# Kernel tuning notes

Measured on AMD Instinct MI355X. Metric: run time of the kernel, lower is better.

Reference implementation:

```python
import jax, jax.numpy as jnp
import numpy as np
from jax import lax

NH = 8  # heads


def _ln(x, g, b):
    m = x.mean(-1, keepdims=True)
    v = ((x - m) ** 2).mean(-1, keepdims=True)
    return (x - m) * lax.rsqrt(v + 1e-5) * g + b


def _pos_idx(n):
    # torch: linspace(n-1,0,n)[:,None] + linspace(0,n-1,n)[None,:], flattened long
    r = np.linspace(n - 1, 0, n).reshape(n, 1)
    c = np.linspace(0, n - 1, n).reshape(1, n)
    return jnp.asarray((r + c).reshape(-1).astype(np.int32))


def _mha(q_in, k_in, v_in, in_w, in_b, out_w, out_b, pos_enc=None, pos_idx=None, attn_mask=None):
    # MultiheadAttentionRelative: q/k/v proj + relative pos-encoding gather terms
    w, bsz, e = q_in.shape
    hd = e // NH
    scale = hd ** -0.5
    q = (q_in @ in_w[:e].T + in_b[:e]) * scale
    k = k_in @ in_w[e:2 * e].T + in_b[e:2 * e]
    v = v_in @ in_w[2 * e:].T + in_b[2 * e:]
    q = q.reshape(w, bsz, NH, hd)
    k = k.reshape(w, bsz, NH, hd)
    v = v.reshape(w, bsz, NH, hd)
    attn = jnp.einsum('wnec,vnec->newv', q, k)  # [N,E,W,W']
    if pos_enc is not None:
        pe = pos_enc[pos_idx].reshape(w, w, e)  # [2W-1,C] -> [W,W',C] gather
        q_r = ((pe @ in_w[:e].T + in_b[:e]) * scale).reshape(w, w, NH, hd)
        k_r = (pe @ in_w[e:2 * e].T + in_b[e:2 * e]).reshape(w, w, NH, hd)
        attn = attn + jnp.einsum('wnec,wvec->newv', q, k_r) + jnp.einsum('vnec,wvec->newv', k, q_r)
    if attn_mask is not None:
        attn = attn + attn_mask[None, None]
    raw = attn
    p = jax.nn.softmax(attn, axis=-1)
    v_o = jnp.einsum('newv,vnec->wnec', p, v).reshape(w, bsz, e)
    return v_o @ out_w.T + out_b, raw.sum(axis=1)


def _interp_lin(x, out_size):
    # torch F.interpolate(mode='linear', align_corners=False) along last axis
    L_in = x.shape[-1]
    if L_in == out_size:
        return x
    coords = jnp.clip((jnp.arange(out_size, dtype=jnp.float32) + 0.5) * (L_in / out_size) - 0.5, 0.0, L_in - 1.0)
    lo = jnp.floor(coords).astype(jnp.int32)
    hi = jnp.minimum(lo + 1, L_in - 1)
    frac = coords - lo.astype(jnp.float32)
    return x[..., lo] * (1.0 - frac) + x[..., hi] * frac


def _conv(x, w, b, pad):
    y = lax.conv_general_dilated(x, w, (1, 1), pad, dimension_numbers=('NCHW', 'OIHW', 'NCHW'))
    return y + b[None, :, None, None]


def _self_layer(feat, feat1, pos, pidx, pos1, pidx1, posy, pidxy, posy1, pidxy1, p):
    iw, ib, ow, ob, n1g, n1b, n2g, n2b = p
    f2 = _ln(feat, n1g, n1b)
    f4 = _ln(feat1, n2g, n2b)
    w_, h2, c = f2.shape
    w1_, h4, c1 = f4.shape
    # row<->col switch: [W,2HN,C] -> [HN,2W,C]
    f2y = jnp.transpose(f2.reshape(w_, 2, h2 // 2, c), (2, 1, 0, 3)).reshape(h2 // 2, 2 * w_, c)
    f4y = jnp.transpose(f4.reshape(w1_, 2, h4 // 2, c1), (2, 1, 0, 3)).reshape(h4 // 2, 2 * w1_, c1)
    f2y, _ = _mha(f2y, f2y, f2y, iw[1], ib[1], ow[1], ob[1], posy, pidxy)
    f2 = jnp.transpose(f2y.reshape(h2 // 2, 2, w_, c), (2, 1, 0, 3)).reshape(w_, h2, c)
    f4y, _ = _mha(f4y, f4y, f4y, iw[3], ib[3], ow[3], ob[3], posy1, pidxy1)
    f4 = jnp.transpose(f4y.reshape(h4 // 2, 2, w1_, c1), (2, 1, 0, 3)).reshape(w1_, h4, c1)
    f2, _ = _mha(f2, f2, f2, iw[0], ib[0], ow[0], ob[0], pos, pidx)
    f4, _ = _mha(f4, f4, f4, iw[2], ib[2], ow[2], ob[2], pos1, pidx1)
    return feat + f2, feat1 + f4


def _cross_layer(fl, fr, fl1, fr1, pos, pidx, pos1, pidx1, p, last):
    iw, ib, ow, ob, n1g, n1b, n2g, n2b, mw1, mb1, mw2, mb2 = p
    fl2 = _ln(fl, n1g, n1b)
    fr2 = _ln(fr, n1g, n1b)
    fl4 = _ln(fl1, n2g, n2b)
    fr4 = _ln(fr1, n2g, n2b)
    up_r, _ = _mha(fr2, fl2, fl2, iw[0], ib[0], ow[0], ob[0], jnp.flip(pos, 0), pidx)
    up_r1, _ = _mha(fr4, fl4, fl4, iw[1], ib[1], ow[1], ob[1], jnp.flip(pos1, 0), pidx1)
    fr = fr + up_r
    fr1n = fr1 + up_r1
    if last:
        w = fl2.shape[0]
        w1 = fl4.shape[0]
        m = jnp.where(jnp.triu(jnp.ones((w, w), jnp.float32), 1) == 1.0, -jnp.inf, 0.0)
        m1 = jnp.where(jnp.triu(jnp.ones((w1, w1), jnp.float32), 1) == 1.0, -jnp.inf, 0.0)
    else:
        m = None
        m1 = None
    fr2n = _ln(fr, n1g, n1b)
    up_l, raw = _mha(fl2, fr2n, fr2n, iw[0], ib[0], ow[0], ob[0], pos, pidx, m)
    fr4n = _ln(fr1n, n2g, n2b)
    up_l1, _ = _mha(fl4, fr4n, fr4n, iw[1], ib[1], ow[1], ob[1], pos1, pidx1, m1)
    fl = fl + up_l
    fl1n = fl1 + up_l1
    feat = jnp.concatenate([fl, fr], 1)        # [W,2HN,C]
    feat_n = jnp.concatenate([fl1n, fr1n], 1)  # [W1,2HN,C]
    x = jnp.transpose(feat_n, (2, 1, 0))       # [C,2HN,W1]
    x = _interp_lin(x, feat.shape[0])          # [C,2HN,W]
    feat_n = jnp.transpose(x, (2, 1, 0))
    feat_n = jnp.concatenate([feat_n, feat], 2)  # [W,2HN,2C]
    x = jnp.transpose(feat_n, (2, 1, 0))[None]   # [1,2C,2HN,W]
    x = _conv(x, mw1, mb1, 'VALID')
    x = _conv(x, mw2, mb2, ((1, 1), (1, 1)))
    out = jnp.transpose(x[0], (2, 1, 0))         # [W,2HN,C]
    return out, raw


def reference(feat_left, feat_right, feat_left1, feat_right1, pos_enc, pos_enc1, pos_enc_y, pos_enc_y1,
              sa_in_w, sa_in_b, sa_out_w, sa_out_b, sa_n1_g, sa_n1_b, sa_n2_g, sa_n2_b,
              ca_in_w, ca_in_b, ca_out_w, ca_out_b, ca_n1_g, ca_n1_b, ca_n2_g, ca_n2_b,
              merge_w1, merge_b1, merge_w2, merge_b2):
    bs, c, h, w = feat_left.shape
    w1 = feat_left1.shape[3]
    hn = h * bs

    def flat(x):
        return jnp.transpose(x, (3, 2, 0, 1)).reshape(x.shape[3], -1, c)  # [W,HN,C]

    fl, fr = flat(feat_left), flat(feat_right)
    fl1, fr1 = flat(feat_left1), flat(feat_right1)
    pidx = _pos_idx(w)
    pidx1 = _pos_idx(w1)
    pidxy = _pos_idx(hn)
    pidxy1 = _pos_idx(hn)
    feat = jnp.concatenate([fl, fr], 1)    # [W,2HN,C]
    feat1 = jnp.concatenate([fl1, fr1], 1)  # [W1,2HN,C]
    L = sa_in_w.shape[0]
    raw = None
    for i in range(L):
        sp = (sa_in_w[i], sa_in_b[i], sa_out_w[i], sa_out_b[i], sa_n1_g[i], sa_n1_b[i], sa_n2_g[i], sa_n2_b[i])
        feat, feat1 = _self_layer(feat, feat1, pos_enc, pidx, pos_enc1, pidx1, pos_enc_y, pidxy, pos_enc_y1, pidxy1, sp)
        cp = (ca_in_w[i], ca_in_b[i], ca_out_w[i], ca_out_b[i], ca_n1_g[i], ca_n1_b[i], ca_n2_g[i], ca_n2_b[i],
              merge_w1[i], merge_b1[i], merge_w2[i], merge_b2[i])
        feat, raw = _cross_layer(feat[:, :hn], feat[:, hn:], feat1[:, :hn], feat1[:, hn:],
                                 pos_enc, pidx, pos_enc1, pidx1, cp, i == L - 1)
    attn_weight = jnp.transpose(raw.reshape(h, bs, w, w), (1, 0, 2, 3))  # [N,H,W,W]
    return attn_weight


def setup_inputs() -> dict:
    key = jax.random.key(0)
    ks = iter(jax.random.split(key, 40))
    N, C, H, W, W1, Lyr = 1, 128, 64, 128, 64, 6
    s = 0.05
    d = {}
    d['feat_left'] = jax.random.normal(next(ks), (N, C, H, W), jnp.float32)
    d['feat_right'] = jax.random.normal(next(ks), (N, C, H, W), jnp.float32)
    d['feat_left1'] = jax.random.normal(next(ks), (N, C, H, W1), jnp.float32)
    d['feat_right1'] = jax.random.normal(next(ks), (N, C, H, W1), jnp.float32)
    d['pos_enc'] = jax.random.normal(next(ks), (2 * W - 1, C), jnp.float32) * 0.1
    d['pos_enc1'] = jax.random.normal(next(ks), (2 * W1 - 1, C), jnp.float32) * 0.1
    d['pos_enc_y'] = jax.random.normal(next(ks), (2 * H - 1, C), jnp.float32) * 0.1
    d['pos_enc_y1'] = jax.random.normal(next(ks), (2 * H - 1, C), jnp.float32) * 0.1
    d['sa_in_w'] = jax.random.normal(next(ks), (Lyr, 4, 3 * C, C), jnp.float32) * s
    d['sa_in_b'] = jnp.zeros((Lyr, 4, 3 * C), jnp.float32)
    d['sa_out_w'] = jax.random.normal(next(ks), (Lyr, 4, C, C), jnp.float32) * s
    d['sa_out_b'] = jnp.zeros((Lyr, 4, C), jnp.float32)
    d['sa_n1_g'] = jnp.ones((Lyr, C), jnp.float32)
    d['sa_n1_b'] = jnp.zeros((Lyr, C), jnp.float32)
    d['sa_n2_g'] = jnp.ones((Lyr, C), jnp.float32)
    d['sa_n2_b'] = jnp.zeros((Lyr, C), jnp.float32)
    d['ca_in_w'] = jax.random.normal(next(ks), (Lyr, 2, 3 * C, C), jnp.float32) * s
    d['ca_in_b'] = jnp.zeros((Lyr, 2, 3 * C), jnp.float32)
    d['ca_out_w'] = jax.random.normal(next(ks), (Lyr, 2, C, C), jnp.float32) * s
    d['ca_out_b'] = jnp.zeros((Lyr, 2, C), jnp.float32)
    d['ca_n1_g'] = jnp.ones((Lyr, C), jnp.float32)
    d['ca_n1_b'] = jnp.zeros((Lyr, C), jnp.float32)
    d['ca_n2_g'] = jnp.ones((Lyr, C), jnp.float32)
    d['ca_n2_b'] = jnp.zeros((Lyr, C), jnp.float32)
    d['merge_w1'] = jax.random.normal(next(ks), (Lyr, 128, 256, 1, 1), jnp.float32) * s
    d['merge_b1'] = jnp.zeros((Lyr, 128), jnp.float32)
    d['merge_w2'] = jax.random.normal(next(ks), (Lyr, 128, 128, 3, 3), jnp.float32) * s
    d['merge_b2'] = jnp.zeros((Lyr, 128), jnp.float32)
    return d
```

## Files before the change

### kernel.cpp

```cpp
#include <hip/hip_runtime.h>
#include <hip/hip_bf16.h>
#include <math.h>


typedef __attribute__((ext_vector_type(8))) short bf16x8;
typedef __attribute__((ext_vector_type(4))) float f32x4;
typedef __hip_bfloat16 bf16;

__device__ __forceinline__ float b2f(unsigned short u) {
  return __uint_as_float((unsigned)u << 16);
}
__device__ __forceinline__ short f2bs(float x) {
  bf16 h = __float2bfloat16(x);
  short s;
  __builtin_memcpy(&s, &h, 2);
  return s;
}
__device__ __forceinline__ int ymap(int t, int D0, int D1) {
  return (t % D0) * (2 * D1) + ((t / D0) & 1) * D1 + t / (2 * D0);
}


__global__ void k_build_feat(const float* __restrict__ L, const float* __restrict__ R,
                             float* __restrict__ feat, int W) {
  int t = blockIdx.x;
  int c = threadIdx.x;
  int b = t & 127;
  int w = t >> 7;
  const float* src = (b < 64) ? L : R;
  int h = b & 63;
  feat[(size_t)t * 128 + c] = src[((size_t)c * 64 + h) * W + w];
}

struct FDesc { const float* s; bf16* d; int n; };
struct FArgs { FDesc d[9]; int cum[10]; int nprob; };
__global__ void k_f2b_multi(FArgs fa) {
  int bid = blockIdx.x;
  int p = 0;
  while (p + 1 < fa.nprob && bid >= fa.cum[p + 1]) ++p;
  const FDesc d = fa.d[p];
  int i = (bid - fa.cum[p]) * 1024 + threadIdx.x * 4;
  if (i + 3 < d.n) {
    float4 x = *(const float4*)(d.s + i);
    d.d[i + 0] = __float2bfloat16(x.x);
    d.d[i + 1] = __float2bfloat16(x.y);
    d.d[i + 2] = __float2bfloat16(x.z);
    d.d[i + 3] = __float2bfloat16(x.w);
  } else {
    for (int z = 0; z < 4 && i + z < d.n; ++z) d.d[i + z] = __float2bfloat16(d.s[i + z]);
  }
}

__global__ void k_wfullb(const float* __restrict__ w2, bf16* __restrict__ wf) {
  int bid = blockIdx.x;
  int l = bid >> 7, co = bid & 127;
  int ci = threadIdx.x;
  const float* src = w2 + (size_t)l * 128 * 128 * 9;
  bf16* dst = wf + (size_t)l * 128 * 1152;
#pragma unroll
  for (int ky = 0; ky < 3; ky++)
#pragma unroll
    for (int kx = 0; kx < 3; kx++)
      dst[(size_t)co * 1152 + (kx * 3 + ky) * 128 + ci] =
          __float2bfloat16(src[((size_t)(co * 128 + ci) * 3 + ky) * 3 + kx]);
}

__global__ void k_zero_guard(bf16* p0, bf16* p1) {
  int t = threadIdx.x;
  p0[255 * 256 + t] = __float2bfloat16(0.0f);
  p1[127 * 256 + t] = __float2bfloat16(0.0f);
}

__global__ void k_rawcomb4(const float* __restrict__ A, const float* __restrict__ B2,
                           const float* __restrict__ C3, const float* __restrict__ D4,
                           bf16* __restrict__ out) {
  int i = blockIdx.x * 256 + threadIdx.x;
  int v = i & 127, w = (i >> 7) & 127;
  float rv = (v > w) ? 0.0f : (A[i] + B2[i] + C3[i] + D4[i]);
  out[i] = __float2bfloat16(rv);
}


struct LDesc { const float* src; bf16* dst; const float* g; const float* be;
               int ntok, Bout, PBin, offIn; };
struct LArgs { LDesc d[4]; int cum[5]; int nprob; };

__global__ __launch_bounds__(256) void k_ln_multi(LArgs la) {
  int bid = blockIdx.x;
  int p = 0;
  while (p + 1 < la.nprob && bid >= la.cum[p + 1]) ++p;
  const LDesc d = la.d[p];
  int t = (bid - la.cum[p]) * 4 + (threadIdx.x >> 6);
  int lane = threadIdx.x & 63;
  if (t >= d.ntok) return;
  int w = t / d.Bout, b = t - w * d.Bout;
  const float* row = d.src + (size_t)(w * d.PBin + d.offIn + b) * 128;
  float x0 = row[lane], x1 = row[lane + 64];
  float s = x0 + x1;
#pragma unroll
  for (int o = 32; o; o >>= 1) s += __shfl_xor(s, o, 64);
  float m = s * (1.0f / 128.0f);
  float d0 = x0 - m, d1 = x1 - m;
  float v = d0 * d0 + d1 * d1;
#pragma unroll
  for (int o = 32; o; o >>= 1) v += __shfl_xor(v, o, 64);
  float r = 1.0f / sqrtf(v * (1.0f / 128.0f) + 1e-5f);
  bf16* orow = d.dst + (size_t)t * 128;
  orow[lane]      = __float2bfloat16(d0 * r * d.g[lane]      + d.be[lane]);
  orow[lane + 64] = __float2bfloat16(d1 * r * d.g[lane + 64] + d.be[lane + 64]);
}


struct GDesc {
  const bf16* A; const float* Af0; const float* Af1;
  const bf16* W; const float* bias;
  bf16* Cb; float* Cf; const float* resid;
  int M, N, K, lda, scaleN;
  int imode, iD0, iD1;
  int omode, oD0, oD1, ooff;
};
struct GArgs { GDesc d[6]; int cum[7]; int nprob; };

__global__ __launch_bounds__(256) void k_gemm_multi(GArgs ga) {
  __shared__ bf16x8 sA[64 * 4];
  __shared__ bf16x8 sB[64 * 4];
  int bid = blockIdx.x;
  int p = 0;
  while (p + 1 < ga.nprob && bid >= ga.cum[p + 1]) ++p;
  const GDesc d = ga.d[p];
  int local = bid - ga.cum[p];
  int tilesx = d.N >> 6;
  int ty = local / tilesx, tx = local - ty * tilesx;
  const int m0 = ty << 6, n0 = tx << 6;
  const int tid = threadIdx.x;
  const int lane = tid & 63;
  const int wave = tid >> 6;
  const int wm = wave >> 1, wn = wave & 1;
  const int fr = lane & 15;
  const int kc = lane >> 4;
  f32x4 acc[2][2];
#pragma unroll
  for (int f = 0; f < 2; f++)
#pragma unroll
    for (int g = 0; g < 2; g++) acc[f][g] = (f32x4){0.f, 0.f, 0.f, 0.f};

  for (int k0 = 0; k0 < d.K; k0 += 32) {
    {
      int row = tid >> 2, ch = tid & 3;
      int m = m0 + row;
      bf16x8 val = (bf16x8){0, 0, 0, 0, 0, 0, 0, 0};
      if (d.imode == 0) {
        if (m < d.M) val = *(const bf16x8*)(d.A + (size_t)m * d.lda + k0 + ch * 8);
      } else if (d.imode == 1) {
        if (m < d.M) {
          int ar = ymap(m, d.iD0, d.iD1);
          val = *(const bf16x8*)(d.A + (size_t)ar * d.lda + k0 + ch * 8);
        }
      } else if (d.imode == 2) {
        int kblk = k0 >> 7;
        int kx = kblk / 3, ky = kblk - kx * 3;
        int arow = m + (kx - 1) * 128;
        int y = (m & 127) + (ky - 1);
        if (arow >= 0 && arow < d.M && y >= 0 && y < 128)
          val = *(const bf16x8*)(d.A + (size_t)arow * d.lda + (k0 & 127) + ch * 8);
      } else {
        int kk = k0 + ch * 8;
        int w = m >> 7, y = m & 127;
        if (kk < 128) {
          float xo = fminf(fmaxf(w * 0.5f - 0.25f, 0.0f), 63.0f);
          int lo = (int)xo;
          int hi = (lo + 1 < 63) ? lo + 1 : 63;
          float f = xo - (float)lo;
          const float* a0 = d.Af0 + ((size_t)lo * 128 + y) * 128 + kk;
          const float* a1 = d.Af0 + ((size_t)hi * 128 + y) * 128 + kk;
#pragma unroll
          for (int z = 0; z < 8; ++z) val[z] = f2bs(a0[z] * (1.0f - f) + a1[z] * f);
        } else {
          const float* a0 = d.Af1 + (size_t)m * 128 + (kk - 128);
#pragma unroll
          for (int z = 0; z < 8; ++z) val[z] = f2bs(a0[z]);
        }
      }
      sA[row * 4 + (ch ^ ((row >> 2) & 3))] = val;
      bf16x8 bval = *(const bf16x8*)(d.W + (size_t)(n0 + row) * d.K + k0 + ch * 8);
      sB[row * 4 + (ch ^ ((row >> 2) & 3))] = bval;
    }
    __syncthreads();
    bf16x8 af[2], bg[2];
#pragma unroll
    for (int f = 0; f < 2; ++f) {
      int row = wm * 32 + f * 16 + fr;
      af[f] = sA[row * 4 + (kc ^ ((row >> 2) & 3))];
    }
#pragma unroll
    for (int g = 0; g < 2; ++g) {
      int row = wn * 32 + g * 16 + fr;
      bg[g] = sB[row * 4 + (kc ^ ((row >> 2) & 3))];
    }
#pragma unroll
    for (int f = 0; f < 2; ++f)
#pragma unroll
      for (int g = 0; g < 2; ++g)
        acc[f][g] = __builtin_amdgcn_mfma_f32_16x16x32_bf16(af[f], bg[g], acc[f][g], 0, 0, 0);
    __syncthreads();
  }
  const int r4 = (lane >> 4) << 2;
  const int ocol = lane & 15;
#pragma unroll
  for (int f = 0; f < 2; ++f) {
#pragma unroll
    for (int g = 0; g < 2; ++g) {
      int n = n0 + wn * 32 + g * 16 + ocol;
      float bv = d.bias ? d.bias[n] : 0.0f;
      bool sc = (n < d.scaleN);
#pragma unroll
      for (int i = 0; i < 4; ++i) {
        int m = m0 + wm * 32 + f * 16 + r4 + i;
        if (m < d.M) {
          int row;
          if (d.omode == 0) row = (m / d.oD0) * d.oD1 + d.ooff + (m % d.oD0);
          else row = ymap(m, d.oD0, d.oD1);
          size_t idx = (size_t)row * d.N + n;
          float val = acc[f][g][i] + bv;
          if (sc) val *= 0.25f;
          if (d.resid) val += d.resid[idx];
          if (d.Cb) d.Cb[idx] = __float2bfloat16(val);
          else d.Cf[idx] = val;
        }
      }
    }
  }
}


struct ADesc {
  const bf16* Q; const bf16* K; const bf16* V;
  const bf16* PPb; bf16* O;
  float* raw0; float* raw1; float* raw2; float* raw3;
  int ldQ, ldK, ldV, Wlen, B, sflip, useMask;
};
struct AArgs { ADesc d[2]; int cum[3]; int nprob; };

template<int WLEN, int SGN>
__device__ __forceinline__ void attn_core(const ADesc& d, int b, int st, int h,
                                          int tid, bf16* Vt, bf16* Pl, bf16* T2l,
                                          bf16* Ost) {
  constexpr int NT = WLEN / 16;
  constexpr int R = WLEN - 1;
  const f32x4 z4 = (f32x4){0.f, 0.f, 0.f, 0.f};
  const bf16x8 zb = (bf16x8){0, 0, 0, 0, 0, 0, 0, 0};

  {
    int q = tid & (WLEN / 2 - 1);
    int cc = tid >> ((WLEN == 128) ? 6 : 5);
    constexpr int CH = (WLEN == 128) ? 16 : 8;
    int cb = cc * CH;
    const bf16* v0p = d.V + ((size_t)(2 * q) * d.B + b) * d.ldV + h * 64 + cb;
    const bf16* v1p = d.V + ((size_t)(2 * q + 1) * d.B + b) * d.ldV + h * 64 + cb;
#pragma unroll
    for (int j = 0; j < CH; j += 8) {
      bf16x8 a = *(const bf16x8*)(v0p + j);
      bf16x8 bb = *(const bf16x8*)(v1p + j);
#pragma unroll
      for (int z = 0; z < 8; ++z) {
        unsigned pk = (unsigned)(unsigned short)a[z] |
                      ((unsigned)(unsigned short)bb[z] << 16);
        *(unsigned*)(Vt + (size_t)(cb + j + z) * 136 + 2 * q) = pk;
      }
    }
  }
  __syncthreads();

  const int wave = tid >> 6, l = tid & 63;
  const int lm = l & 15, lg = l >> 4;
  const bool zlane = (lg >= 2);
  bf16* Pw  = Pl + wave * (16 * 136);
  bf16* T2w = T2l + wave * (16 * 20);
  int p0[4], src[4], hi[4], tsel[4];
  bool csel[4];
#pragma unroll
  for (int i = 0; i < 4; ++i) {
    p0[i] = SGN * (lm - 4 * lg - i) + 15;
    src[i] = (l & 48) | (p0[i] & 15);
    hi[i] = p0[i] & 16;
    if (SGN == 1) {
      int t0 = lm + 15 - 4 * lg - i;
      csel[i] = (t0 < 16);
      tsel[i] = csel[i] ? t0 : t0 - 16;
    } else {
      int t0 = lm - 15 + 4 * lg + i;
      csel[i] = (t0 >= 0);
      tsel[i] = csel[i] ? t0 : t0 + 16;
    }
  }

  const int w0 = st * 16;
  const int chb = h * 64 + wave * 16 + lg * 8;

  bf16x8 qf = zb;
  if (!zlane) qf = *(const bf16x8*)(d.Q + ((size_t)(w0 + lm) * d.B + b) * d.ldQ + chb);

  const int U0 = (SGN == 1) ? (R - w0 - 15) : (R + w0 - WLEN + 1);
  const int Ub0 = (SGN == 1) ? (R - w0 - 15) : (R - (WLEN - 16) + w0 - 15);
  const bf16* t1p = d.PPb + (size_t)(U0 + lm) * 256 + 128 + chb;
  const bf16* t2p = d.PPb + (size_t)(Ub0 + lm) * 256 + chb;
  const int v0i = ((SGN == 1) ? 0 : (WLEN - 16)) + lm;
  const bf16* kp = d.K + ((size_t)v0i * d.B + b) * d.ldK + chb;
  const ptrdiff_t kstep = (ptrdiff_t)SGN * 16 * d.B * d.ldK;

  f32x4 t1a;
  {
    bf16x8 z = zb;
    if (!zlane) z = *(const bf16x8*)t1p;
    t1p += 16 * 256;
    t1a = __builtin_amdgcn_mfma_f32_16x16x32_bf16(qf, z, z4, 0, 0, 0);
  }
  int v = v0i;
#pragma unroll
  for (int j = 0; j < NT; ++j) {
    f32x4 t1b;
    {
      bf16x8 z = zb;
      if (!zlane) z = *(const bf16x8*)t1p;
      t1p += 16 * 256;
      t1b = __builtin_amdgcn_mfma_f32_16x16x32_bf16(qf, z, z4, 0, 0, 0);
    }
    bf16x8 kf = zb;
    if (!zlane) kf = *(const bf16x8*)kp;
    kp += kstep;
    f32x4 s4 = __builtin_amdgcn_mfma_f32_16x16x32_bf16(qf, kf, z4, 0, 0, 0);
    bf16x8 zA = zb, zB = zb;
    if (!zlane) {
      zA = *(const bf16x8*)t2p;
      zB = *(const bf16x8*)(t2p + 16 * 256);
    }
    t2p += 16 * 256;
    f32x4 t2A = __builtin_amdgcn_mfma_f32_16x16x32_bf16(zA, kf, z4, 0, 0, 0);
    f32x4 t2B = __builtin_amdgcn_mfma_f32_16x16x32_bf16(zB, kf, z4, 0, 0, 0);
#pragma unroll
    for (int i = 0; i < 4; ++i)
      T2w[lm * 20 + tsel[i]] = f2bs(csel[i] ? t2A[i] : t2B[i]);
    ushort4 t2u = *(const ushort4*)(T2w + lm * 20 + 4 * lg);
    unsigned short t2a[4] = {t2u.x, t2u.y, t2u.z, t2u.w};
#pragma unroll
    for (int i = 0; i < 4; ++i) {
      float va = __shfl(t1a[i], src[i], 64);
      float vb = __shfl(t1b[i], src[i], 64);
      float s = s4[i] + (hi[i] ? vb : va) + b2f(t2a[i]);
      Pw[(4 * lg + i) * 136 + v] = f2bs(__expf(s));
    }
    t1a = t1b;
    v += SGN * 16;
  }
  const bf16x8 ones = (bf16x8){0x3F80, 0x3F80, 0x3F80, 0x3F80,
                               0x3F80, 0x3F80, 0x3F80, 0x3F80};
  f32x4 oa = z4, rsm = z4;
#pragma unroll
  for (int vc = 0; vc < NT / 2; ++vc) {
    bf16x8 pf = *(const bf16x8*)(Pw + lm * 136 + vc * 32 + lg * 8);
    bf16x8 vf = *(const bf16x8*)(Vt + (size_t)(wave * 16 + lm) * 136 + vc * 32 + lg * 8);
    oa = __builtin_amdgcn_mfma_f32_16x16x32_bf16(pf, vf, oa, 0, 0, 0);
    rsm = __builtin_amdgcn_mfma_f32_16x16x32_bf16(pf, ones, rsm, 0, 0, 0);
  }
#pragma unroll
  for (int i = 0; i < 4; ++i)
    Ost[(4 * lg + i) * 80 + wave * 16 + lm] = f2bs(oa[i] / rsm[i]);
  __syncthreads();
  if (tid < 128) {
    int row = tid >> 3, ch8 = (tid & 7) * 8;
    bf16x8 vv = *(const bf16x8*)(Ost + row * 80 + ch8);
    *(bf16x8*)(d.O + ((size_t)(w0 + row) * d.B + b) * 128 + h * 64 + ch8) = vv;
  }
}

__global__ __launch_bounds__(256, 4) void k_attn_mfma(AArgs aa) {
  __shared__ bf16 Vt[64 * 136];
  __shared__ bf16 Pl[4 * 16 * 136];
  __shared__ bf16 T2l[4 * 16 * 20];
  __shared__ bf16 Ost[16 * 80];
  int bid = blockIdx.x;
  int p = 0;
  while (p + 1 < aa.nprob && bid >= aa.cum[p + 1]) ++p;
  const ADesc d = aa.d[p];
  int local = bid - aa.cum[p];
  int b = local % d.B;
  int rest = local / d.B;
  int ns = d.Wlen >> 4;
  int st = rest % ns, h = rest / ns;
  int tid = threadIdx.x;
  if (d.Wlen == 128) {
    if (d.sflip == 1) attn_core<128, 1>(d, b, st, h, tid, Vt, Pl, T2l, Ost);
    else attn_core<128, -1>(d, b, st, h, tid, Vt, Pl, T2l, Ost);
  } else {
    if (d.sflip == 1) attn_core<64, 1>(d, b, st, h, tid, Vt, Pl, T2l, Ost);
    else attn_core<64, -1>(d, b, st, h, tid, Vt, Pl, T2l, Ost);
  }
}

__global__ __launch_bounds__(256, 2) void k_attn_raw(ADesc d) {
  __shared__ bf16 T2l[4 * 16 * 20];
  constexpr int NT = 8;
  constexpr int R = 127;
  const f32x4 z4 = (f32x4){0.f, 0.f, 0.f, 0.f};
  const bf16x8 zb = (bf16x8){0, 0, 0, 0, 0, 0, 0, 0};
  int bid = blockIdx.x;
  int b = bid % d.B, st = bid / d.B;
  int tid = threadIdx.x;
  const int wave = tid >> 6, l = tid & 63;
  const int lm = l & 15, lg = l >> 4;
  const bool zlane = (lg >= 2);
  bf16* T2w = T2l + wave * (16 * 20);
  int p0[4];
#pragma unroll
  for (int i = 0; i < 4; ++i) p0[i] = (lm - 4 * lg - i) + 15;
  const int w0 = st * 16;
  f32x4 raw[NT];
#pragma unroll
  for (int vt = 0; vt < NT; ++vt) raw[vt] = z4;

  for (int hh = 0; hh < 2; ++hh) {
    const int e = wave * 2 + hh;
    const int chb = e * 16 + lg * 8;
    bf16x8 qf = zb;
    if (!zlane) qf = *(const bf16x8*)(d.Q + ((size_t)(w0 + lm) * d.B + b) * d.ldQ + chb);
    const int U0 = R - w0 - 15;
    f32x4 t1a;
    {
      int u = min(max(U0 + lm, 0), 2 * R);
      bf16x8 z = zb;
      if (!zlane) z = *(const bf16x8*)(d.PPb + (size_t)u * 256 + 128 + chb);
      t1a = __builtin_amdgcn_mfma_f32_16x16x32_bf16(qf, z, z4, 0, 0, 0);
    }
#pragma unroll
    for (int j = 0; j < NT; ++j) {
      const int vt = j;
      const int v = vt * 16 + lm;
      f32x4 t1b;
      {
        int u = min(max(U0 + (j + 1) * 16 + lm, 0), 2 * R);
        bf16x8 z = zb;
        if (!zlane) z = *(const bf16x8*)(d.PPb + (size_t)u * 256 + 128 + chb);
        t1b = __builtin_amdgcn_mfma_f32_16x16x32_bf16(qf, z, z4, 0, 0, 0);
      }
      bf16x8 kf = zb;
      if (!zlane) kf = *(const bf16x8*)(d.K + ((size_t)v * d.B + b) * d.ldK + chb);
      f32x4 s4 = __builtin_amdgcn_mfma_f32_16x16x32_bf16(qf, kf, z4, 0, 0, 0);
      const int Ub = R + vt * 16 - w0 - 15;
#pragma unroll
      for (int u2 = 0; u2 < 2; ++u2) {
        int ua = min(max(Ub + u2 * 16 + lm, 0), 2 * R);
        bf16x8 z = zb;
        if (!zlane) z = *(const bf16x8*)(d.PPb + (size_t)ua * 256 + chb);
        f32x4 t2 = __builtin_amdgcn_mfma_f32_16x16x32_bf16(z, kf, z4, 0, 0, 0);
#pragma unroll
        for (int i = 0; i < 4; ++i) {
          int u = Ub + u2 * 16 + 4 * lg + i;
          int t = R + v - u - w0;
          if (t >= 0 && t < 16) T2w[lm * 20 + t] = f2bs(t2[i]);
        }
      }
      ushort4 t2u = *(const ushort4*)(T2w + lm * 20 + 4 * lg);
      unsigned short t2a[4] = {t2u.x, t2u.y, t2u.z, t2u.w};
#pragma unroll
      for (int i = 0; i < 4; ++i) {
        int src = (l & 48) | (p0[i] & 15);
        float va = __shfl(t1a[i], src, 64);
        float vb = __shfl(t1b[i], src, 64);
        float s = s4[i] + ((p0[i] & 16) ? vb : va) + b2f(t2a[i]);
        if (v > (w0 + 4 * lg + i)) s = -INFINITY;
        raw[vt][i] += s;
      }
      t1a = t1b;
    }
  }
  float* rp = (wave == 0) ? d.raw0 : (wave == 1) ? d.raw1 : (wave == 2) ? d.raw2 : d.raw3;
#pragma unroll
  for (int vt = 0; vt < NT; ++vt)
#pragma unroll
    for (int i = 0; i < 4; ++i)
      rp[((size_t)b * 128 + (w0 + 4 * lg + i)) * 128 + vt * 16 + lm] = raw[vt][i];
}


extern "C" void kernel_launch(void* const* d_in, const int* in_sizes, int n_in,
                              void* d_out, int out_size, void* d_ws, size_t ws_size,
                              hipStream_t stream) {
  (void)in_sizes; (void)n_in; (void)out_size; (void)ws_size;
  const float* FLt  = (const float*)d_in[0];
  const float* FRt  = (const float*)d_in[1];
  const float* FL1t = (const float*)d_in[2];
  const float* FR1t = (const float*)d_in[3];
  const float* PE   = (const float*)d_in[4];
  const float* PE1  = (const float*)d_in[5];
  const float* PEY  = (const float*)d_in[6];
  const float* PEY1 = (const float*)d_in[7];
  const float* SA_IW = (const float*)d_in[8];
  const float* SA_IB = (const float*)d_in[9];
  const float* SA_OW = (const float*)d_in[10];
  const float* SA_OB = (const float*)d_in[11];
  const float* SA_N1G = (const float*)d_in[12];
  const float* SA_N1B = (const float*)d_in[13];
  const float* SA_N2G = (const float*)d_in[14];
  const float* SA_N2B = (const float*)d_in[15];
  const float* CA_IW = (const float*)d_in[16];
  const float* CA_IB = (const float*)d_in[17];
  const float* CA_OW = (const float*)d_in[18];
  const float* CA_OB = (const float*)d_in[19];
  const float* CA_N1G = (const float*)d_in[20];
  const float* CA_N1B = (const float*)d_in[21];
  const float* CA_N2G = (const float*)d_in[22];
  const float* CA_N2B = (const float*)d_in[23];
  const float* MW1 = (const float*)d_in[24];
  const float* MB1 = (const float*)d_in[25];
  const float* MW2 = (const float*)d_in[26];
  const float* MB2 = (const float*)d_in[27];

  float* ws = (float*)d_ws;
  float* FEAT  = ws;
  float* FEAT1 = ws + 2097152;
  float* FN2   = ws + 3145728;
  bf16* PP0b   = (bf16*)(ws + 4194304);
  bf16* PP1b   = (bf16*)(ws + 4259840);
  bf16* hb = (bf16*)(ws + 4292608);
  bf16* QKV   = hb;
  bf16* QKV1  = hb + 6291456;
  bf16* Xb    = hb + 9437184;
  bf16* XBb   = hb + 11534336;
  bf16* Ob    = hb + 12582912;
  bf16* Ob1   = hb + 14680064;
  bf16* PEb   = hb + 15728640;
  bf16* PE1b  = hb + 15761408;
  bf16* PEYb  = hb + 15777792;
  bf16* PEY1b = hb + 15794176;
  bf16* SAIWb = hb + 15810560;
  bf16* SAOWb = hb + 18169856;
  bf16* CAIWb = hb + 18563072;
  bf16* CAOWb = hb + 19742720;
  bf16* MW1b  = hb + 19939328;
  bf16* WFb   = hb + 20135936;

  bf16* QR   = QKV + 3145728;
  bf16* FL4F = QKV + 4194304;
  bf16* QR1  = QKV + 5767168;
  bf16* KVq  = QKV1;
  bf16* KVq1 = QKV1 + 2097152;
  bf16* XR2  = Xb;
  bf16* XR21 = Xb + 1048576;

  GArgs ga; int ng = 0; int gb = 0;
  auto gadd = [&](GDesc gd) { ga.cum[ng] = gb; ga.d[ng] = gd;
                              gb += ((gd.M + 63) >> 6) * (gd.N >> 6); ++ng; };
  auto gflush = [&]() { ga.nprob = ng;
                        k_gemm_multi<<<gb, 256, 0, stream>>>(ga); ng = 0; gb = 0; };
  LArgs la; int nl = 0; int lb = 0;
  auto lnadd = [&](LDesc ld) { la.cum[nl] = lb; la.d[nl] = ld;
                               lb += (ld.ntok + 3) / 4; ++nl; };
  auto lnflush = [&]() { la.nprob = nl;
                         k_ln_multi<<<lb, 256, 0, stream>>>(la); nl = 0; lb = 0; };
  AArgs aa; int na = 0; int ab = 0;
  auto aadd = [&](ADesc ad) { aa.cum[na] = ab; aa.d[na] = ad;
                              ab += ad.B * (ad.Wlen >> 4) * 2; ++na; };
  auto aflush = [&]() { aa.nprob = na;
                        k_attn_mfma<<<ab, 256, 0, stream>>>(aa); na = 0; ab = 0; };

  auto G = [&](const bf16* A, const bf16* W, const float* bias,
               bf16* Cb, float* Cf, const float* resid,
               int M, int N, int K, int lda, int scaleN,
               int imode, int iD0, int iD1,
               int omode, int oD0, int oD1, int ooff,
               const float* Af0 = nullptr, const float* Af1 = nullptr) {
    GDesc gd; gd.A = A; gd.Af0 = Af0; gd.Af1 = Af1; gd.W = W; gd.bias = bias;
    gd.Cb = Cb; gd.Cf = Cf; gd.resid = resid;
    gd.M = M; gd.N = N; gd.K = K; gd.lda = lda; gd.scaleN = scaleN;
    gd.imode = imode; gd.iD0 = iD0; gd.iD1 = iD1;
    gd.omode = omode; gd.oD0 = oD0; gd.oD1 = oD1; gd.ooff = ooff;
    gadd(gd);
  };
  auto AT = [&](const bf16* Q, int ldQ, const bf16* K, int ldK, const bf16* V, int ldV,
                const bf16* PPb, int Wlen, int B, int sflip, bf16* O) {
    ADesc ad; ad.Q = Q; ad.K = K; ad.V = V; ad.PPb = PPb; ad.O = O;
    ad.raw0 = nullptr; ad.raw1 = nullptr; ad.raw2 = nullptr; ad.raw3 = nullptr;
    ad.ldQ = ldQ; ad.ldK = ldK; ad.ldV = ldV; ad.Wlen = Wlen; ad.B = B;
    ad.sflip = sflip; ad.useMask = 0;
    aadd(ad);
  };

  {
    FArgs fa; int nf = 0; int fb = 0;
    auto fadd = [&](const float* s, bf16* dd, int n) {
      fa.cum[nf] = fb; fa.d[nf] = FDesc{s, dd, n}; fb += (n + 1023) / 1024; ++nf; };
    fadd(SA_IW, SAIWb, 6 * 4 * 384 * 128);
    fadd(SA_OW, SAOWb, 6 * 4 * 128 * 128);
    fadd(CA_IW, CAIWb, 6 * 2 * 384 * 128);
    fadd(CA_OW, CAOWb, 6 * 2 * 128 * 128);
    fadd(MW1,   MW1b,  6 * 128 * 256);
    fadd(PE,    PEb,   255 * 128);
    fadd(PE1,   PE1b,  127 * 128);
    fadd(PEY,   PEYb,  127 * 128);
    fadd(PEY1,  PEY1b, 127 * 128);
    fa.nprob = nf;
    k_f2b_multi<<<fb, 256, 0, stream>>>(fa);
  }
  k_wfullb<<<768, 128, 0, stream>>>(MW2, WFb);
  k_zero_guard<<<1, 256, 0, stream>>>(PP0b, PP1b);
  k_build_feat<<<16384, 128, 0, stream>>>(FLt, FRt, FEAT, 128);
  k_build_feat<<<8192, 128, 0, stream>>>(FL1t, FR1t, FEAT1, 64);

  for (int l = 0; l < 6; ++l) {
    bool last = (l == 5);
    const bf16* iw  = SAIWb + (size_t)l * 4 * 384 * 128;
    const float* ib = SA_IB + (size_t)l * 4 * 384;
    const bf16* ow  = SAOWb + (size_t)l * 4 * 128 * 128;
    const float* ob = SA_OB + (size_t)l * 4 * 128;
    const bf16* ciw  = CAIWb + (size_t)l * 2 * 384 * 128;
    const float* cib = CA_IB + (size_t)l * 2 * 384;
    const bf16* cow  = CAOWb + (size_t)l * 2 * 128 * 128;
    const float* cob = CA_OB + (size_t)l * 2 * 128;
    const bf16* ciw1 = ciw + 384 * 128;
    const float* cib1 = cib + 384;
    const bf16* cow1 = cow + 128 * 128;
    const float* cob1 = cob + 128;
    const int IW = 384 * 128, OW = 128 * 128;

    lnadd(LDesc{FEAT, Xb, SA_N1G + l * 128, SA_N1B + l * 128, 16384, 128, 128, 0});
    if (!last) lnadd(LDesc{FEAT1, XBb, SA_N2G + l * 128, SA_N2B + l * 128, 8192, 128, 128, 0});
    lnflush();
    G(Xb, iw + IW, ib + 384, QKV, nullptr, nullptr, 16384, 384, 128, 128, 128, 1, 128, 64, 0, 1, 1, 0);
    if (!last) G(XBb, iw + 3 * IW, ib + 3 * 384, QKV1, nullptr, nullptr, 8192, 384, 128, 128, 128, 1, 64, 64, 0, 1, 1, 0);
    G(PEYb, iw + IW, ib + 384, PP0b, nullptr, nullptr, 127, 256, 128, 128, 128, 0, 0, 0, 0, 1, 1, 0);
    if (!last) G(PEY1b, iw + 3 * IW, ib + 3 * 384, PP1b, nullptr, nullptr, 127, 256, 128, 128, 128, 0, 0, 0, 0, 1, 1, 0);
    gflush();
    AT(QKV, 384, QKV + 128, 384, QKV + 256, 384, PP0b, 64, 256, 1, Ob);
    if (!last) AT(QKV1, 384, QKV1 + 128, 384, QKV1 + 256, 384, PP1b, 64, 128, 1, Ob1);
    aflush();
    G(Ob, ow + OW, ob + 128, Xb, nullptr, nullptr, 16384, 128, 128, 128, 0, 0, 0, 0, 1, 128, 64, 0);
    if (!last) G(Ob1, ow + 3 * OW, ob + 3 * 128, XBb, nullptr, nullptr, 8192, 128, 128, 128, 0, 0, 0, 0, 1, 64, 64, 0);
    gflush();
    G(Xb, iw, ib, QKV, nullptr, nullptr, 16384, 384, 128, 128, 128, 0, 0, 0, 0, 1, 1, 0);
    if (!last) G(XBb, iw + 2 * IW, ib + 2 * 384, QKV1, nullptr, nullptr, 8192, 384, 128, 128, 128, 0, 0, 0, 0, 1, 1, 0);
    G(PEb, iw, ib, PP0b, nullptr, nullptr, 255, 256, 128, 128, 128, 0, 0, 0, 0, 1, 1, 0);
    if (!last) G(PE1b, iw + 2 * IW, ib + 2 * 384, PP1b, nullptr, nullptr, 127, 256, 128, 128, 128, 0, 0, 0, 0, 1, 1, 0);
    gflush();
    AT(QKV, 384, QKV + 128, 384, QKV + 256, 384, PP0b, 128, 128, 1, Ob);
    if (!last) AT(QKV1, 384, QKV1 + 128, 384, QKV1 + 256, 384, PP1b, 64, 128, 1, Ob1);
    aflush();
    G(Ob, ow, ob, nullptr, FEAT, FEAT, 16384, 128, 128, 128, 0, 0, 0, 0, 0, 1, 1, 0);
    if (!last) G(Ob1, ow + 2 * OW, ob + 2 * 128, nullptr, FEAT1, FEAT1, 8192, 128, 128, 128, 0, 0, 0, 0, 0, 1, 1, 0);
    gflush();

    lnadd(LDesc{FEAT, Xb, CA_N1G + l * 128, CA_N1B + l * 128, 8192, 64, 128, 0});
    lnadd(LDesc{FEAT, Xb + 1048576, CA_N1G + l * 128, CA_N1B + l * 128, 8192, 64, 128, 64});
    if (!last) {
      lnadd(LDesc{FEAT1, XBb, CA_N2G + l * 128, CA_N2B + l * 128, 4096, 64, 128, 0});
      lnadd(LDesc{FEAT1, XBb + 524288, CA_N2G + l * 128, CA_N2B + l * 128, 4096, 64, 128, 64});
    }
    lnflush();
    G(Xb, ciw, cib, QKV, nullptr, nullptr, 8192, 384, 128, 128, 128, 0, 0, 0, 0, 1, 1, 0);
    G(Xb + 1048576, ciw, cib, QR, nullptr, nullptr, 8192, 128, 128, 128, 128, 0, 0, 0, 0, 1, 1, 0);
    if (!last) {
      G(XBb, ciw1, cib1, FL4F, nullptr, nullptr, 4096, 384, 128, 128, 128, 0, 0, 0, 0, 1, 1, 0);
      G(XBb + 524288, ciw1, cib1, QR1, nullptr, nullptr, 4096, 128, 128, 128, 128, 0, 0, 0, 0, 1, 1, 0);
    }
    G(PEb, ciw, cib, PP0b, nullptr, nullptr, 255, 256, 128, 128, 128, 0, 0, 0, 0, 1, 1, 0);
    if (!last) G(PE1b, ciw1, cib1, PP1b, nullptr, nullptr, 127, 256, 128, 128, 128, 0, 0, 0, 0, 1, 1, 0);
    gflush();
    AT(QR, 128, QKV + 128, 384, QKV + 256, 384, PP0b, 128, 64, -1, Ob);
    if (!last) AT(QR1, 128, FL4F + 128, 384, FL4F + 256, 384, PP1b, 64, 64, -1, Ob1);
    aflush();
    G(Ob, cow, cob, nullptr, FEAT, FEAT, 8192, 128, 128, 128, 0, 0, 0, 0, 0, 64, 128, 64);
    if (!last) G(Ob1, cow1, cob1, nullptr, FN2, FEAT1, 4096, 128, 128, 128, 0, 0, 0, 0, 0, 64, 128, 64);
    gflush();
    lnadd(LDesc{FEAT, XR2, CA_N1G + l * 128, CA_N1B + l * 128, 8192, 64, 128, 64});
    if (!last) lnadd(LDesc{FN2, XR21, CA_N2G + l * 128, CA_N2B + l * 128, 4096, 64, 128, 64});
    lnflush();
    G(XR2, ciw + 128 * 128, cib + 128, KVq, nullptr, nullptr, 8192, 256, 128, 128, 0, 0, 0, 0, 0, 1, 1, 0);
    if (!last) G(XR21, ciw1 + 128 * 128, cib1 + 128, KVq1, nullptr, nullptr, 4096, 256, 128, 128, 0, 0, 0, 0, 0, 1, 1, 0);
    gflush();
    if (last) {
      ADesc ad; ad.Q = QKV; ad.K = KVq; ad.V = KVq + 128; ad.PPb = PP0b;
      ad.O = nullptr;
      ad.raw0 = FEAT1; ad.raw1 = FN2; ad.raw2 = (float*)Ob; ad.raw3 = (float*)FL4F;
      ad.ldQ = 384; ad.ldK = 256; ad.ldV = 256;
      ad.Wlen = 128; ad.B = 64; ad.sflip = 1; ad.useMask = 1;
      k_attn_raw<<<64 * 8, 256, 0, stream>>>(ad);
      k_rawcomb4<<<4096, 256, 0, stream>>>(FEAT1, FN2, (float*)Ob, (float*)FL4F,
                                           (bf16*)d_out);
      break;
    }
    AT(QKV, 384, KVq, 256, KVq + 128, 256, PP0b, 128, 64, 1, Ob);
    AT(FL4F, 384, KVq1, 256, KVq1 + 128, 256, PP1b, 64, 64, 1, Ob1);
    aflush();
    G(Ob, cow, cob, nullptr, FEAT, FEAT, 8192, 128, 128, 128, 0, 0, 0, 0, 0, 64, 128, 0);
    G(Ob1, cow1, cob1, nullptr, FN2, FEAT1, 4096, 128, 128, 128, 0, 0, 0, 0, 0, 64, 128, 0);
    gflush();
    G(nullptr, MW1b + (size_t)l * 128 * 256, MB1 + l * 128, Ob, nullptr, nullptr,
      16384, 128, 256, 256, 0, 3, 0, 0, 0, 1, 1, 0, FN2, FEAT);
    gflush();
    G(Ob, WFb + (size_t)l * 128 * 1152, MB2 + l * 128, nullptr, FEAT, nullptr,
      16384, 128, 1152, 128, 0, 2, 0, 0, 0, 1, 1, 0);
    gflush();
  }
}
```

Baseline: 1.634 ms.

## Fold self-attention output projection into next in-projection via precomputed combined weights

Precomputes per-layer combined weights W_in·W_out and biases W_in·b_out + b_in, so the output projection GEMM followed by the next input projection becomes a single GEMM from attention output straight to QKV. This removes one GEMM launch batch and the intermediate Xb write and read per layer. It adds small setup kernels and changes rounding, because the combined weights are stored in bf16. It relies on no residual or norm sitting between the two projections, which the original chain G(Ob→Xb) then G(Xb→QKV) suggests.

```diff
diff --git a/kernel.cpp b/kernel.cpp
--- a/kernel.cpp
+++ b/kernel.cpp
@@ -69,6 +69,40 @@
   int t = threadIdx.x;
   p0[255 * 256 + t] = __float2bfloat16(0.0f);
   p1[127 * 256 + t] = __float2bfloat16(0.0f);
+}
+
+struct WCArgs { const bf16* iw[12]; const bf16* ow[12]; bf16* out[12]; };
+__global__ __launch_bounds__(256) void k_wcomb(WCArgs a) {
+  __shared__ bf16 sOw[128 * 128];
+  int p = blockIdx.x / 6, rc = blockIdx.x % 6;
+  const bf16* iw = a.iw[p];
+  const bf16* ow = a.ow[p];
+  for (int i = threadIdx.x; i < 128 * 16; i += 256)
+    ((bf16x8*)sOw)[i] = ((const bf16x8*)ow)[i];
+  __syncthreads();
+  int row = rc * 64 + (threadIdx.x >> 2);
+  int seg = (threadIdx.x & 3) * 32;
+  float acc[32];
+#pragma unroll
+  for (int c = 0; c < 32; ++c) acc[c] = 0.f;
+  for (int t = 0; t < 128; ++t) {
+    float av = b2f((unsigned short)iw[row * 128 + t]);
+#pragma unroll
+    for (int c = 0; c < 32; ++c)
+      acc[c] = fmaf(av, b2f((unsigned short)sOw[t * 128 + seg + c]), acc[c]);
+  }
+  bf16* o = a.out[p] + (size_t)row * 128 + seg;
+  for (int c = 0; c < 32; ++c) o[c] = __float2bfloat16(acc[c]);
+}
+
+struct BCArgs { const float* iwf[12]; const float* obf[12]; const float* ibf[12]; float* out[12]; };
+__global__ void k_bcomb(BCArgs a) {
+  int p = blockIdx.x, j = threadIdx.x;
+  const float* iw = a.iwf[p] + (size_t)j * 128;
+  const float* ob = a.obf[p];
+  float acc = a.ibf[p][j];
+  for (int t = 0; t < 128; ++t) acc = fmaf(iw[t], ob[t], acc);
+  a.out[p][j] = acc;
 }
 
 __global__ void k_rawcomb4(const float* __restrict__ A, const float* __restrict__ B2,
@@ -521,6 +555,7 @@
   float* FN2   = ws + 3145728;
   bf16* PP0b   = (bf16*)(ws + 4194304);
   bf16* PP1b   = (bf16*)(ws + 4259840);
+  float* B2f   = ws + 4276224;
   bf16* hb = (bf16*)(ws + 4292608);
   bf16* QKV   = hb;
   bf16* QKV1  = hb + 6291456;
@@ -538,6 +573,7 @@
   bf16* CAOWb = hb + 19742720;
   bf16* MW1b  = hb + 19939328;
   bf16* WFb   = hb + 20135936;
+  bf16* W2b   = hb + 21020672;
 
   bf16* QR   = QKV + 3145728;
   bf16* FL4F = QKV + 4194304;
@@ -603,6 +639,25 @@
   }
   k_wfullb<<<768, 128, 0, stream>>>(MW2, WFb);
   k_zero_guard<<<1, 256, 0, stream>>>(PP0b, PP1b);
+  {
+    WCArgs wc; BCArgs bc;
+    for (int l = 0; l < 6; ++l) {
+      for (int s = 0; s < 2; ++s) {
+        int p = l * 2 + s;
+        int iwi = (s == 0) ? 0 : 2;
+        int owi = (s == 0) ? 1 : 3;
+        wc.iw[p]  = SAIWb + (size_t)l * 4 * 384 * 128 + (size_t)iwi * 384 * 128;
+        wc.ow[p]  = SAOWb + (size_t)l * 4 * 128 * 128 + (size_t)owi * 128 * 128;
+        wc.out[p] = W2b + (size_t)p * 384 * 128;
+        bc.iwf[p] = SA_IW + (size_t)l * 4 * 384 * 128 + (size_t)iwi * 384 * 128;
+        bc.obf[p] = SA_OB + (size_t)l * 4 * 128 + (size_t)owi * 128;
+        bc.ibf[p] = SA_IB + (size_t)l * 4 * 384 + (size_t)iwi * 384;
+        bc.out[p] = B2f + (size_t)p * 384;
+      }
+    }
+    k_wcomb<<<72, 256, 0, stream>>>(wc);
+    k_bcomb<<<12, 384, 0, stream>>>(bc);
+  }
   k_build_feat<<<16384, 128, 0, stream>>>(FLt, FRt, FEAT, 128);
   k_build_feat<<<8192, 128, 0, stream>>>(FL1t, FR1t, FEAT1, 64);
 
@@ -633,11 +688,10 @@
     AT(QKV, 384, QKV + 128, 384, QKV + 256, 384, PP0b, 64, 256, 1, Ob);
     if (!last) AT(QKV1, 384, QKV1 + 128, 384, QKV1 + 256, 384, PP1b, 64, 128, 1, Ob1);
     aflush();
-    G(Ob, ow + OW, ob + 128, Xb, nullptr, nullptr, 16384, 128, 128, 128, 0, 0, 0, 0, 1, 128, 64, 0);
-    if (!last) G(Ob1, ow + 3 * OW, ob + 3 * 128, XBb, nullptr, nullptr, 8192, 128, 128, 128, 0, 0, 0, 0, 1, 64, 64, 0);
-    gflush();
-    G(Xb, iw, ib, QKV, nullptr, nullptr, 16384, 384, 128, 128, 128, 0, 0, 0, 0, 1, 1, 0);
-    if (!last) G(XBb, iw + 2 * IW, ib + 2 * 384, QKV1, nullptr, nullptr, 8192, 384, 128, 128, 128, 0, 0, 0, 0, 1, 1, 0);
+    G(Ob, W2b + (size_t)(l * 2) * 49152, B2f + (l * 2) * 384, QKV, nullptr, nullptr,
+      16384, 384, 128, 128, 128, 1, 64, 128, 0, 1, 1, 0);
+    if (!last) G(Ob1, W2b + (size_t)(l * 2 + 1) * 49152, B2f + (l * 2 + 1) * 384, QKV1,
+                 nullptr, nullptr, 8192, 384, 128, 128, 128, 1, 64, 64, 0, 1, 1, 0);
     G(PEb, iw, ib, PP0b, nullptr, nullptr, 255, 256, 128, 128, 128, 0, 0, 0, 0, 1, 1, 0);
     if (!last) G(PE1b, iw + 2 * IW, ib + 2 * 384, PP1b, nullptr, nullptr, 127, 256, 128, 128, 128, 0, 0, 0, 0, 1, 1, 0);
     gflush();
```

Result: no change. 1.617 ms, median of 2 (-1.0%).
